# Performance work log

Hardware: AMD Instinct MI355X
Metric: run time of the kernel (lower is better)

## Reference

```python
import jax, jax.numpy as jnp
import numpy as np

B, L, K = 4, 2048, 30
NS, NV = 1024, 256   # node hidden (scalar, vector)
ES, EV = 32, 1       # edge hidden (scalar, vector)
CLAMP = 32           # clamp_rel_pos
PE = 16              # num positional embeddings

def _nan_to_num(t):
    return jnp.where(jnp.isfinite(t), t, jnp.zeros((), t.dtype))

def _norm(t, axis=-1, keepdims=False, eps=1e-8):
    return jnp.sqrt(jnp.sum(t * t, axis=axis, keepdims=keepdims) + eps)

def _normalize(t, axis=-1):
    return _nan_to_num(t / _norm(t, axis=axis, keepdims=True))

def _norm_no_nan(t, axis=-1, keepdims=False, eps=1e-8, sqrt=True):
    out = jnp.maximum(jnp.sum(t * t, axis=axis, keepdims=keepdims), eps)
    return jnp.sqrt(out) if sqrt else out

def _rbf(values, v_min, v_max, n_bins=16):
    centers = jnp.linspace(v_min, v_max, n_bins)
    std = (v_max - v_min) / n_bins
    z = (values[..., None] - centers) / std
    return jnp.exp(-z * z)

def _dihedrals(X, eps=1e-7):
    b = X.shape[0]
    Xf = X[:, :, :3].reshape(b, -1, 3)           # [B, 3L, 3]
    U = _normalize(Xf[:, 1:] - Xf[:, :-1])
    u2, u1, u0 = U[:, :-2], U[:, 1:-1], U[:, 2:]
    n2 = _normalize(jnp.cross(u2, u1))
    n1 = _normalize(jnp.cross(u1, u0))
    cosD = jnp.clip(jnp.sum(n2 * n1, -1), -1 + eps, 1 - eps)
    D = jnp.sign(jnp.sum(u2 * n1, -1)) * jnp.arccos(cosD)
    D = jnp.pad(D, ((0, 0), (1, 2))).reshape(b, -1, 3)
    return jnp.concatenate([jnp.cos(D), jnp.sin(D)], -1)   # [B,L,6]

def _orientations(Xca):
    f = jnp.pad(_normalize(Xca[:, 1:] - Xca[:, :-1]), ((0, 0), (0, 1), (0, 0)))
    bk = jnp.pad(_normalize(Xca[:, :-1] - Xca[:, 1:]), ((0, 0), (1, 0), (0, 0)))
    return jnp.concatenate([f[:, :, None], bk[:, :, None]], -2)  # [B,L,2,3]

def _sidechains(X):
    n, origin, c = X[:, :, 0], X[:, :, 1], X[:, :, 2]
    c, n = _normalize(c - origin), _normalize(n - origin)
    bisector = _normalize(c + n)
    perp = _normalize(jnp.cross(c, n))
    return -bisector * float(np.sqrt(1.0 / 3.0)) - perp * float(np.sqrt(2.0 / 3.0))

def _dist(Xca, coord_mask, res_idx, padding_mask, k, order=3):
    n = Xca.shape[1]
    cmf = coord_mask.astype(jnp.float32)
    cm2 = cmf[:, None, :] * cmf[:, :, None]
    rmf = (~padding_mask).astype(jnp.float32)
    rm2 = rmf[:, None, :] * rmf[:, :, None]
    dX = Xca[:, None, :, :] - Xca[:, :, None, :]
    D = cm2 * _norm(dX, axis=-1)
    cov = (jnp.abs(res_idx[:, :, None] - res_idx[:, None, :]) <= order).astype(jnp.float32)
    D_cov = D * (1.0 - cov)
    seqpos = jnp.arange(n)
    Dseq = jnp.abs(seqpos[:, None] - seqpos[None, :]).astype(jnp.float32)
    D_adjust = _nan_to_num(D_cov) + (1.0 - cm2) * (1e8 + Dseq * 1e6) + (1.0 - rm2) * 1e10
    _, E_idx = jax.lax.top_k(-D_adjust, k)                # k smallest
    D_neighbors = jnp.take_along_axis(D, E_idx, axis=-1)  # regather raw D (as in source)
    return D_neighbors, E_idx, D_neighbors < 5e7, D_neighbors < 5e9

def _edge_features(coords, coord_mask, res_idx, padding_mask):
    Xca = coords[:, :, 1]
    E_dist, E_idx, E_cm, E_rm = _dist(Xca, coord_mask, res_idx, padding_mask, K)
    b, n, k = E_idx.shape
    src = jnp.broadcast_to(jnp.arange(n, dtype=E_idx.dtype)[None, :, None], (b, n, k))
    edge_index = jnp.stack([src, E_idx], 0).reshape(2, b, n * k)
    E_dist = E_dist.reshape(b, n * k)
    E_cm = E_cm.reshape(b, n * k)
    E_rm = E_rm.reshape(b, n * k)
    E_cmf = E_cm[..., None].astype(jnp.float32)
    edge_start = jnp.take_along_axis(res_idx, edge_index[0], axis=-1)
    edge_end = jnp.take_along_axis(res_idx, edge_index[1], axis=-1)
    d = jnp.clip(edge_start - edge_end, -CLAMP, CLAMP).astype(jnp.float32)
    freq = jnp.exp(jnp.arange(0, PE, 2, dtype=jnp.float32) * (-np.log(10000.0) / PE))
    ang = d[..., None] * freq
    pos = jnp.concatenate([jnp.cos(ang), jnp.sin(ang)], -1)
    D_rbf = _rbf(E_dist, 0.0, 20.0)
    X_src = jnp.broadcast_to(Xca[:, :, None, :], (b, n, k, 3)).reshape(b, n * k, 3)
    X_dest = jnp.take_along_axis(Xca, edge_index[1][..., None], axis=1)
    cm_src = jnp.broadcast_to(coord_mask[:, :, None], (b, n, k)).reshape(b, n * k)
    cm_dest = jnp.take_along_axis(coord_mask, edge_index[1], axis=1)
    E_vec = X_src - X_dest
    E_mean = jnp.sum(E_vec * E_cmf, 1, keepdims=True) / jnp.sum(E_cmf, 1, keepdims=True)
    E_vec = E_vec * E_cmf + E_mean * (1.0 - E_cmf)
    edge_s = _nan_to_num(jnp.concatenate([D_rbf, pos], -1))
    edge_v = _nan_to_num(_normalize(E_vec)[:, :, None, :])
    edge_s = jnp.concatenate([edge_s,
                              (~cm_src).astype(jnp.float32)[..., None],
                              (~cm_dest).astype(jnp.float32)[..., None]], -1)  # [B,Lk,34]
    invalid = (~E_rm) | (~E_cm)   # remove_edges_without_coords=True
    edge_index = jnp.where(invalid[None], -1, edge_index)
    return edge_s, edge_v, jnp.transpose(edge_index, (1, 0, 2)), invalid

def _gvp(s, v, wh, ws_w, ws_b, wv):
    # v: [..., vi, 3]; activations=(None, None), vector_gate=False
    vh = jnp.einsum('...id,ih->...hd', v, wh)       # [..., h, 3]
    vn = _norm_no_nan(vh, axis=-1)                  # [..., h]
    s_out = jnp.concatenate([s, vn], -1) @ ws_w + ws_b
    v_out = jnp.einsum('...hd,hv->...vd', vh, wv)
    return s_out, v_out

def _gvp_layernorm(s, v, gamma, beta, eps=1e-4):
    mu = jnp.mean(s, -1, keepdims=True)
    var = jnp.mean((s - mu) ** 2, -1, keepdims=True)
    s_out = (s - mu) / jnp.sqrt(var + eps) * gamma + beta
    vn2 = _norm_no_nan(v, axis=-1, keepdims=True, sqrt=False)
    v_out = v / jnp.sqrt(jnp.mean(vn2, axis=-2, keepdims=True))
    return s_out, v_out

def _forward(coords, coord_mask, res_idx, padding_mask, confidence,
             node_wh, node_ws_w, node_ws_b, node_wv, node_ln_g, node_ln_b,
             edge_wh, edge_ws_w, edge_ws_b, edge_wv, edge_ln_g, edge_ln_b,
             conf_w, conf_b):
    node_s = jnp.concatenate([_dihedrals(coords),
                              coord_mask.astype(jnp.float32)[..., None]], -1)  # [B,L,7]
    node_v = jnp.concatenate([_orientations(coords[:, :, 1]),
                              _sidechains(coords)[:, :, None]], -2)            # [B,L,3,3]
    edge_s, edge_v, edge_index, invalid = _edge_features(coords, coord_mask, res_idx, padding_mask)
    # torch.no_grad() over featurization
    node_s, node_v, edge_s, edge_v = map(jax.lax.stop_gradient,
                                         (node_s, node_v, edge_s, edge_v))
    ns, nv = _gvp_layernorm(*_gvp(node_s, node_v, node_wh, node_ws_w, node_ws_b, node_wv),
                            node_ln_g, node_ln_b)
    es, ev = _gvp_layernorm(*_gvp(edge_s, edge_v, edge_wh, edge_ws_w, edge_ws_b, edge_wv),
                            edge_ln_g, edge_ln_b)
    ns = ns + _rbf(confidence, 0.0, 1.0) @ conf_w + conf_b
    b = ns.shape[0]
    ns = ns.reshape(b * L, NS)
    nv = nv.reshape(b * L, NV, 3)
    es = es.reshape(b * L * K, ES)
    ev = ev.reshape(b * L * K, EV, 3)
    # flatten_graph (padded: invalid edges kept with index -1, embeddings zeroed)
    valid = (~invalid).reshape(-1)
    ei = edge_index + (jnp.arange(b, dtype=edge_index.dtype) * L)[:, None, None]
    ei = jnp.transpose(ei, (1, 0, 2)).reshape(2, -1)
    ei = jnp.where(valid[None, :], ei, -1)
    es = jnp.where(valid[:, None], es, 0.0)
    ev = jnp.where(valid[:, None, None], ev, 0.0)
    return ns, nv, es, ev, ei

def setup_inputs():
    key = jax.random.key(0)
    ks = jax.random.split(key, 12)
    def lin(k, fan_in, shape):
        return jax.random.normal(k, shape, jnp.float32) / np.sqrt(fan_in)
    return {
        'coords': jax.random.normal(ks[0], (B, L, 3, 3), jnp.float32),
        'coord_mask': jax.random.randint(ks[1], (B, L), 0, 2) > 0,
        'res_idx': jnp.arange(B * L, dtype=jnp.int32).reshape(B, L),
        'padding_mask': jnp.zeros((B, L), dtype=bool),
        'confidence': jax.random.uniform(ks[2], (B, L), jnp.float32),
        'node_wh': lin(ks[3], 3, (3, NV)),
        'node_ws_w': lin(ks[4], NV + 7, (NV + 7, NS)),
        'node_ws_b': jnp.zeros((NS,), jnp.float32),
        'node_wv': lin(ks[5], NV, (NV, NV)),
        'node_ln_g': jnp.ones((NS,), jnp.float32),
        'node_ln_b': jnp.zeros((NS,), jnp.float32),
        'edge_wh': lin(ks[6], 1, (1, 1)),
        'edge_ws_w': lin(ks[7], 35, (35, ES)),
        'edge_ws_b': jnp.zeros((ES,), jnp.float32),
        'edge_wv': lin(ks[8], 1, (1, 1)),
        'edge_ln_g': jnp.ones((ES,), jnp.float32),
        'edge_ln_b': jnp.zeros((ES,), jnp.float32),
        'conf_w': lin(ks[9], 16, (16, NS)),
        'conf_b': jnp.zeros((NS,), jnp.float32),
    }

def reference(coords, coord_mask, res_idx, padding_mask, confidence,
              node_wh, node_ws_w, node_ws_b, node_wv, node_ln_g, node_ln_b,
              edge_wh, edge_ws_w, edge_ws_b, edge_wv, edge_ln_g, edge_ln_b,
              conf_w, conf_b):
    return _forward(coords, coord_mask, res_idx, padding_mask, confidence,
                    node_wh, node_ws_w, node_ws_b, node_wv, node_ln_g, node_ln_b,
                    edge_wh, edge_ws_w, edge_ws_b, edge_wv, edge_ln_g, edge_ln_b,
                    conf_w, conf_b)
```

## Files before the change

### kernel.cpp

```cpp
#include <hip/hip_runtime.h>
#include <math.h>

constexpr int Bc = 4, Lc = 2048, Kc = 30;
constexpr int Nn = Bc * Lc;
constexpr int NSc = 1024, NVc = 256;
constexpr int NEc = Nn * Kc;
constexpr int SK = 263;

constexpr size_t OUT_NS = 0;
constexpr size_t OUT_NV = (size_t)Nn * NSc;
constexpr size_t OUT_ES = OUT_NV + (size_t)Nn * NVc * 3;
constexpr size_t OUT_EV = OUT_ES + (size_t)NEc * 32;
constexpr size_t OUT_EI = OUT_EV + (size_t)NEc * 3;

constexpr size_t WS_SIN = 0;
constexpr size_t WS_NDV = WS_SIN + (size_t)Nn * SK;
constexpr size_t WS_EIX = WS_NDV + (size_t)Nn * 9;
constexpr size_t WS_EDS = WS_EIX + (size_t)NEc;
constexpr size_t WS_CMF = WS_EDS + (size_t)NEc;

__device__ __forceinline__ void norml3(float& x, float& y, float& z) {
  float ss = x*x + y*y + z*z;
  float inv = 1.0f / sqrtf(ss + 1e-8f);
  x *= inv; y *= inv; z *= inv;
}

__global__ __launch_bounds__(256) void kinit(const unsigned char* __restrict__ cm,
                                             const float* __restrict__ coords,
                                             const int* __restrict__ resid,
                                             const unsigned char* __restrict__ pmask,
                                             const float* __restrict__ wh,
                                             const float* __restrict__ wv,
                                             float* __restrict__ ws,
                                             float4* __restrict__ pack,
                                             float4* __restrict__ whwv4,
                                             float4* __restrict__ wht4) {
  __shared__ float r0[256], r1[256], r2[256];
  __shared__ int flag;
  int tid = threadIdx.x;
  if (blockIdx.x < 32) {
    if (tid == 0) flag = 0;
    __syncthreads();
    int any = 0;
    for (int p = tid; p < 1024; p += 256)
      if (p & 3) any |= cm[p];
    if (any) atomicOr(&flag, 1);
    __syncthreads();
    bool bytefmt = (flag != 0);
    int n = blockIdx.x * 256 + tid;
    unsigned char v = bytefmt ? cm[n] : cm[4*n];
    ws[WS_CMF + n] = v ? 1.f : 0.f;
    int rm = (pmask[n] == 0) ? 1 : 0;
    int w = (resid[n] << 2) | ((v ? 1 : 0) << 1) | rm;
    float4 p;
    p.x = coords[(size_t)n*9 + 3];
    p.y = coords[(size_t)n*9 + 4];
    p.z = coords[(size_t)n*9 + 5];
    p.w = __int_as_float(w);
    pack[n] = p;
  } else {
    int lane = tid & 63, wid = tid >> 6;
    int vcol = (int)(blockIdx.x - 32) * 64 + lane;
    float a0 = 0.f, a1 = 0.f, a2 = 0.f;
    #pragma unroll 4
    for (int hh = 0; hh < 64; ++hh) {
      int h = wid * 64 + hh;
      float wvv = wv[(size_t)h * 256 + vcol];
      a0 = fmaf(wh[h],       wvv, a0);
      a1 = fmaf(wh[256 + h], wvv, a1);
      a2 = fmaf(wh[512 + h], wvv, a2);
    }
    r0[tid] = a0; r1[tid] = a1; r2[tid] = a2;
    __syncthreads();
    if (wid == 0) {
      a0 = r0[lane] + r0[lane+64] + r0[lane+128] + r0[lane+192];
      a1 = r1[lane] + r1[lane+64] + r1[lane+128] + r1[lane+192];
      a2 = r2[lane] + r2[lane+64] + r2[lane+128] + r2[lane+192];
      whwv4[vcol] = float4{a0, a1, a2, 0.f};
    } else if (wid == 1) {
      wht4[vcol] = float4{wh[vcol], wh[256 + vcol], wh[512 + vcol], 0.f};
    }
  }
}

__global__ __launch_bounds__(64) void knode_geom(const float* __restrict__ coords,
                                                 float* __restrict__ ws) {
  int n = blockIdx.x * 64 + threadIdx.x;
  if (n >= Nn) return;
  int b = n / Lc, l = n % Lc;
  const float* Xb = coords + (size_t)b * Lc * 9;
  float ax[7][3];
  #pragma unroll
  for (int m = 0; m < 7; ++m) {
    int t = 3*l + m - 2;
    if (t >= 0 && t < 3*Lc) { ax[m][0]=Xb[t*3+0]; ax[m][1]=Xb[t*3+1]; ax[m][2]=Xb[t*3+2]; }
    else { ax[m][0]=0.f; ax[m][1]=0.f; ax[m][2]=0.f; }
  }
  float U[5][3];
  #pragma unroll
  for (int mi = 0; mi < 5; ++mi) {
    int t = 3*l - 1 + mi;
    if (t >= 0 && t <= 3*Lc - 2) {
      float x = ax[mi+2][0]-ax[mi+1][0], y = ax[mi+2][1]-ax[mi+1][1], z = ax[mi+2][2]-ax[mi+1][2];
      norml3(x,y,z);
      U[mi][0]=x; U[mi][1]=y; U[mi][2]=z;
    } else { U[mi][0]=0.f; U[mi][1]=0.f; U[mi][2]=0.f; }
  }
  float cph[3], sph[3];
  #pragma unroll
  for (int a = 0; a < 3; ++a) {
    int t = 3*l + a - 1;
    if (t < 0 || t > 3*Lc - 4) { cph[a] = 1.f; sph[a] = 0.f; continue; }
    const float *u2 = U[a], *u1 = U[a+1], *u0 = U[a+2];
    float n2x = u2[1]*u1[2]-u2[2]*u1[1], n2y = u2[2]*u1[0]-u2[0]*u1[2], n2z = u2[0]*u1[1]-u2[1]*u1[0];
    norml3(n2x,n2y,n2z);
    float n1x = u1[1]*u0[2]-u1[2]*u0[1], n1y = u1[2]*u0[0]-u1[0]*u0[2], n1z = u1[0]*u0[1]-u1[1]*u0[0];
    norml3(n1x,n1y,n1z);
    float cd = n2x*n1x + n2y*n1y + n2z*n1z;
    cd = fminf(fmaxf(cd, -1.f + 1e-7f), 1.f - 1e-7f);
    float dt = u2[0]*n1x + u2[1]*n1y + u2[2]*n1z;
    float sg = (dt > 0.f) ? 1.f : ((dt < 0.f) ? -1.f : 0.f);
    float D = sg * acosf(cd);
    cph[a] = cosf(D); sph[a] = sinf(D);
  }
  float fx=0.f,fy=0.f,fz=0.f, kx=0.f,ky=0.f,kz=0.f;
  if (l < Lc-1) { fx=ax[6][0]-ax[3][0]; fy=ax[6][1]-ax[3][1]; fz=ax[6][2]-ax[3][2]; norml3(fx,fy,fz); }
  if (l > 0)    { kx=ax[0][0]-ax[3][0]; ky=ax[0][1]-ax[3][1]; kz=ax[0][2]-ax[3][2]; norml3(kx,ky,kz); }
  float cx=ax[4][0]-ax[3][0], cy=ax[4][1]-ax[3][1], cz=ax[4][2]-ax[3][2]; norml3(cx,cy,cz);
  float nx=ax[2][0]-ax[3][0], ny=ax[2][1]-ax[3][1], nz=ax[2][2]-ax[3][2]; norml3(nx,ny,nz);
  float bix=cx+nx, biy=cy+ny, biz=cz+nz; norml3(bix,biy,biz);
  float px=cy*nz-cz*ny, py=cz*nx-cx*nz, pz=cx*ny-cy*nx; norml3(px,py,pz);
  const float c1 = 0.57735026f, c2 = 0.81649658f;
  float sx = -bix*c1 - px*c2, sy = -biy*c1 - py*c2, sz = -biz*c1 - pz*c2;

  float cmf = ws[WS_CMF + n];
  float* sr = ws + WS_SIN + (size_t)n * SK;
  sr[0]=cph[0]; sr[1]=cph[1]; sr[2]=cph[2]; sr[3]=sph[0]; sr[4]=sph[1]; sr[5]=sph[2]; sr[6]=cmf;
  float* vr = ws + WS_NDV + (size_t)n * 9;
  vr[0]=fx; vr[1]=fy; vr[2]=fz; vr[3]=kx; vr[4]=ky; vr[5]=kz; vr[6]=sx; vr[7]=sy; vr[8]=sz;
}

__global__ __launch_bounds__(256) void kvnode(const float4* __restrict__ wht4,
                                              const float4* __restrict__ whwv4,
                                              float* __restrict__ ws,
                                              float* __restrict__ out) {
  int tid = threadIdx.x, lane = tid & 63, wid = tid >> 6;
  int n = blockIdx.x * 4 + wid;
  const float* v = ws + WS_NDV + (size_t)n * 9;
  float v00=v[0],v01=v[1],v02=v[2];
  float v10=v[3],v11=v[4],v12=v[5];
  float v20=v[6],v21=v[7],v22=v[8];
  float p = 0.f;
  float vo[4][3];
  #pragma unroll
  for (int m = 0; m < 4; ++m) {
    int h = lane + 64*m;
    float4 wt = wht4[h];
    float vh0 = v00*wt.x + v10*wt.y + v20*wt.z;
    float vh1 = v01*wt.x + v11*wt.y + v21*wt.z;
    float vh2 = v02*wt.x + v12*wt.y + v22*wt.z;
    ws[WS_SIN + (size_t)n*SK + 7 + h] = sqrtf(fmaxf(vh0*vh0 + vh1*vh1 + vh2*vh2, 1e-8f));
    float4 wc = whwv4[h];
    float o0 = v00*wc.x + v10*wc.y + v20*wc.z;
    float o1 = v01*wc.x + v11*wc.y + v21*wc.z;
    float o2 = v02*wc.x + v12*wc.y + v22*wc.z;
    vo[m][0]=o0; vo[m][1]=o1; vo[m][2]=o2;
    p += fmaxf(o0*o0 + o1*o1 + o2*o2, 1e-8f);
  }
  #pragma unroll
  for (int off = 1; off < 64; off <<= 1) p += __shfl_xor(p, off);
  float isd = 1.f / sqrtf(p * (1.f/256.f));
  #pragma unroll
  for (int m = 0; m < 4; ++m) {
    size_t o = OUT_NV + (size_t)n*768 + (size_t)(lane + 64*m)*3;
    out[o+0] = vo[m][0]*isd;
    out[o+1] = vo[m][1]*isd;
    out[o+2] = vo[m][2]*isd;
  }
}

__global__ __launch_bounds__(256) void ktopk(const float4* __restrict__ pack,
                                             float* __restrict__ ws) {
  __shared__ unsigned long long cbuf[4][256];
  int tid = threadIdx.x, lane = tid & 63, wid = tid >> 6;
  int row = blockIdx.x * 4 + wid;
  int b = row >> 11;
  int i = row & (Lc - 1);
  const float4* P = pack + (size_t)b * Lc;
  int* eix = (int*)(ws + WS_EIX);
  unsigned long long lmask_lt = (1ULL << lane) - 1ULL;

  float4 pi = P[i];
  int wi = __float_as_int(pi.w);
  float cmi = ((wi >> 1) & 1) ? 1.f : 0.f;
  float rmi = (wi & 1) ? 1.f : 0.f;
  int ri = wi >> 2;

  unsigned a[32];
  unsigned lmin = 0xFFFFFFFFu;
  #pragma unroll
  for (int m = 0; m < 32; ++m) {
    int j = lane + 64*m;
    float4 pj = P[j];
    int wj = __float_as_int(pj.w);
    float cmj = ((wj >> 1) & 1) ? 1.f : 0.f;
    float rmj = (wj & 1) ? 1.f : 0.f;
    float dx = __fsub_rn(pi.x, pj.x);
    float dy = __fsub_rn(pi.y, pj.y);
    float dz = __fsub_rn(pi.z, pj.z);
    float ss = __fadd_rn(__fadd_rn(__fmul_rn(dx,dx), __fmul_rn(dy,dy)), __fmul_rn(dz,dz));
    float dist = __fsqrt_rn(__fadd_rn(ss, 1e-8f));
    float cm2 = __fmul_rn(cmi, cmj);
    float D = __fmul_rn(cm2, dist);
    int ad = ri - (wj >> 2); ad = ad < 0 ? -ad : ad;
    float covm = (ad <= 3) ? 0.f : 1.f;
    float dseq = (float)(i >= j ? i - j : j - i);
    float t1 = __fmul_rn(__fsub_rn(1.f, cm2), __fadd_rn(1e8f, __fmul_rn(dseq, 1e6f)));
    float rm2 = __fmul_rn(rmi, rmj);
    float t2 = __fmul_rn(__fsub_rn(1.f, rm2), 1e10f);
    float adj = __fadd_rn(__fadd_rn(__fmul_rn(D, covm), t1), t2);
    unsigned u = __float_as_uint(adj);
    a[m] = u;
    lmin = u < lmin ? u : lmin;
  }

  unsigned lo = 0u, hi = 0xFFFFFFFFu;
  while (lo < hi) {
    unsigned mid = lo + ((hi - lo) >> 1);
    unsigned long long bal = __ballot(lmin <= mid);
    if (__popcll(bal) >= Kc) hi = mid; else lo = mid + 1u;
  }
  unsigned Tv = lo;

  unsigned base = 0;
  #pragma unroll
  for (int m = 0; m < 32; ++m) {
    bool pred = (a[m] <= Tv);
    unsigned long long bal = __ballot(pred);
    if (pred) {
      unsigned pos = base + (unsigned)__popcll(bal & lmask_lt);
      if (pos < 256u)
        cbuf[wid][pos] = ((unsigned long long)a[m] << 32) | (unsigned)(lane + 64*m);
    }
    base += (unsigned)__popcll(bal);
  }
  unsigned M = base < 256u ? base : 256u;
  __builtin_amdgcn_wave_barrier();

  for (unsigned idx = (unsigned)lane; idx < M; idx += 64u) {
    unsigned long long k0 = cbuf[wid][idx];
    int rank = 0;
    for (unsigned t = 0; t < M; ++t) rank += (cbuf[wid][t] < k0) ? 1 : 0;
    if (rank < Kc) {
      int j = (int)(k0 & 2047ULL);
      float4 pj = P[j];
      int wj = __float_as_int(pj.w);
      float cmj = ((wj >> 1) & 1) ? 1.f : 0.f;
      float dx = __fsub_rn(pi.x, pj.x);
      float dy = __fsub_rn(pi.y, pj.y);
      float dz = __fsub_rn(pi.z, pj.z);
      float ss2 = __fadd_rn(__fadd_rn(__fmul_rn(dx,dx), __fmul_rn(dy,dy)), __fmul_rn(dz,dz));
      float dist = __fsqrt_rn(__fadd_rn(ss2, 1e-8f));
      float D = __fmul_rn(__fmul_rn(cmi, cmj), dist);
      eix[(size_t)row*Kc + rank] = j;
      ws[WS_EDS + (size_t)row*Kc + rank] = D;
    }
  }
}

__global__ __launch_bounds__(256) void kgemm_s(const float* __restrict__ ws,
                                               const float* __restrict__ wsw,
                                               const float* __restrict__ wsb,
                                               float* __restrict__ out) {
  __shared__ __align__(16) float As[32][132];
  __shared__ __align__(16) float Bs[32][64];
  int tid = threadIdx.x;
  int lb = (int)(blockIdx.x & 7) * 128 + (int)(blockIdx.x >> 3);
  int by = lb >> 4, bx = lb & 15;
  int row0 = by * 128, cn0 = bx * 64;
  int tx = tid & 15, ty = tid >> 4;
  int aka = tid & 15, arw = tid >> 4;
  int bkk = tid >> 4, bc4 = tid & 15;
  const float* Abase = ws + WS_SIN;

  float ar[16];
  float4 br[2];
  #pragma unroll
  for (int h = 0; h < 2; ++h) {
    int ka = h*16 + aka;
    #pragma unroll
    for (int i = 0; i < 8; ++i)
      ar[h*8+i] = Abase[(size_t)(row0 + arw + 16*i)*SK + ka];
    br[h] = *(const float4*)&wsw[(size_t)(h*16 + bkk)*NSc + cn0 + bc4*4];
  }
  float acc[8][4] = {};
  for (int k0 = 0; k0 < SK; k0 += 32) {
    #pragma unroll
    for (int h = 0; h < 2; ++h) {
      #pragma unroll
      for (int i = 0; i < 8; ++i)
        As[h*16 + aka][arw + 16*i] = ar[h*8+i];
      *(float4*)&Bs[h*16 + bkk][bc4*4] = br[h];
    }
    __syncthreads();
    int kn = k0 + 32;
    if (kn < SK) {
      #pragma unroll
      for (int h = 0; h < 2; ++h) {
        int ka = kn + h*16 + aka;
        bool ok = (ka < SK);
        #pragma unroll
        for (int i = 0; i < 8; ++i)
          ar[h*8+i] = ok ? Abase[(size_t)(row0 + arw + 16*i)*SK + ka] : 0.f;
        int kb = kn + h*16 + bkk;
        br[h] = (kb < SK) ? *(const float4*)&wsw[(size_t)kb*NSc + cn0 + bc4*4]
                          : float4{0.f,0.f,0.f,0.f};
      }
    }
    #pragma unroll 4
    for (int kk = 0; kk < 32; ++kk) {
      float4 a0 = *(const float4*)&As[kk][ty*8 + 0];
      float4 a1 = *(const float4*)&As[kk][ty*8 + 4];
      float4 b4 = *(const float4*)&Bs[kk][tx*4];
      float av[8] = {a0.x,a0.y,a0.z,a0.w, a1.x,a1.y,a1.z,a1.w};
      float bv[4] = {b4.x,b4.y,b4.z,b4.w};
      #pragma unroll
      for (int r = 0; r < 8; ++r)
        #pragma unroll
        for (int c = 0; c < 4; ++c)
          acc[r][c] = fmaf(av[r], bv[c], acc[r][c]);
    }
    __syncthreads();
  }
  float4 bb = *(const float4*)&wsb[cn0 + tx*4];
  #pragma unroll
  for (int r = 0; r < 8; ++r) {
    size_t o = OUT_NS + (size_t)(row0 + ty*8 + r)*NSc + cn0 + tx*4;
    float4 ov = {acc[r][0]+bb.x, acc[r][1]+bb.y, acc[r][2]+bb.z, acc[r][3]+bb.w};
    *(float4*)&out[o] = ov;
  }
}

__global__ __launch_bounds__(256) void kedge(const float* __restrict__ coords,
    const int* __restrict__ resid,
    const float* __restrict__ ewh, const float* __restrict__ eww,
    const float* __restrict__ ewb, const float* __restrict__ ewv,
    const float* __restrict__ elg, const float* __restrict__ elb,
    const float* __restrict__ ws, float* __restrict__ out) {
  __shared__ float w[35*32];
  __shared__ float wb[32], g[32], bb[32];
  int tid = threadIdx.x;
  for (int t = tid; t < 35*32; t += 256) w[t] = eww[t];
  if (tid < 32) { wb[tid] = ewb[tid]; g[tid] = elg[tid]; bb[tid] = elb[tid]; }
  __syncthreads();
  int e = blockIdx.x * 256 + tid;
  if (e >= NEc) return;
  int b = e / (Lc*Kc);
  int rem = e - b*(Lc*Kc);
  int i = rem / Kc;
  int row = b*Lc + i;
  const int* eix = (const int*)(ws + WS_EIX);
  int j = eix[e];
  float Dn = ws[WS_EDS + e];
  bool jok = ((unsigned)j < (unsigned)Lc);
  bool valid = jok && (Dn < 5e7f) && (Dn < 5e9f);
  if (!valid) {
    #pragma unroll
    for (int c = 0; c < 32; ++c) out[OUT_ES + (size_t)e*32 + c] = 0.f;
    out[OUT_EV + (size_t)e*3 + 0] = 0.f;
    out[OUT_EV + (size_t)e*3 + 1] = 0.f;
    out[OUT_EV + (size_t)e*3 + 2] = 0.f;
    out[OUT_EI + e]       = -1.f;
    out[OUT_EI + NEc + e] = -1.f;
    return;
  }
  int dcl = resid[row] - resid[b*Lc + j];
  dcl = dcl < -32 ? -32 : (dcl > 32 ? 32 : dcl);
  float dpos = (float)dcl;
  float s[35];
  #pragma unroll
  for (int m = 0; m < 16; ++m) {
    float c = (20.f/15.f) * (float)m;
    float z = (Dn - c) * 0.8f;
    s[m] = expf(-z*z);
  }
  #pragma unroll
  for (int m = 0; m < 8; ++m) {
    float fr = expf((float)(2*m) * (-0.57564627324851148f));
    float ang = dpos * fr;
    s[16+m] = cosf(ang);
    s[24+m] = sinf(ang);
  }
  float csf = ws[WS_CMF + row];
  float cdf = ws[WS_CMF + b*Lc + j];
  s[32] = 1.f - csf; s[33] = 1.f - cdf;
  const float* Xb = coords + (size_t)b*Lc*9;
  float vx = Xb[i*9+3] - Xb[j*9+3];
  float vy = Xb[i*9+4] - Xb[j*9+4];
  float vz = Xb[i*9+5] - Xb[j*9+5];
  float ss2 = vx*vx + vy*vy + vz*vz;
  float inv = 1.f / sqrtf(ss2 + 1e-8f);
  float e0 = vx*inv, e1 = vy*inv, e2 = vz*inv;
  if (!isfinite(e0)) e0 = 0.f;
  if (!isfinite(e1)) e1 = 0.f;
  if (!isfinite(e2)) e2 = 0.f;
  float wh00 = ewh[0], wv00 = ewv[0];
  float vh0 = e0*wh00, vh1 = e1*wh00, vh2 = e2*wh00;
  s[34] = sqrtf(fmaxf(vh0*vh0 + vh1*vh1 + vh2*vh2, 1e-8f));
  float o[32]; float sm = 0.f;
  #pragma unroll
  for (int c = 0; c < 32; ++c) {
    float a = wb[c];
    #pragma unroll
    for (int q = 0; q < 35; ++q) a = fmaf(s[q], w[q*32 + c], a);
    o[c] = a; sm += a;
  }
  float mu = sm * (1.f/32.f);
  float sq = 0.f;
  #pragma unroll
  for (int c = 0; c < 32; ++c) { float dd = o[c]-mu; sq += dd*dd; }
  float isd = 1.f / sqrtf(sq*(1.f/32.f) + 1e-4f);
  float vo0 = vh0*wv00, vo1 = vh1*wv00, vo2 = vh2*wv00;
  float vn2 = fmaxf(vo0*vo0 + vo1*vo1 + vo2*vo2, 1e-8f);
  float ivn = 1.f / sqrtf(vn2);
  #pragma unroll
  for (int c = 0; c < 32; ++c)
    out[OUT_ES + (size_t)e*32 + c] = (o[c]-mu)*isd*g[c] + bb[c];
  out[OUT_EV + (size_t)e*3 + 0] = vo0*ivn;
  out[OUT_EV + (size_t)e*3 + 1] = vo1*ivn;
  out[OUT_EV + (size_t)e*3 + 2] = vo2*ivn;
  out[OUT_EI + e]       = (float)row;
  out[OUT_EI + NEc + e] = (float)(b*Lc + j);
}

__global__ __launch_bounds__(256) void kln_node(const float* __restrict__ conf,
    const float* __restrict__ cw, const float* __restrict__ cb,
    const float* __restrict__ lg, const float* __restrict__ lb,
    float* __restrict__ out) {
  int n = blockIdx.x, tid = threadIdx.x;
  size_t base = OUT_NS + (size_t)n*NSc;
  float x0 = out[base + tid];
  float x1 = out[base + tid + 256];
  float x2 = out[base + tid + 512];
  float x3 = out[base + tid + 768];
  float sm = x0+x1+x2+x3;
  float sq = x0*x0+x1*x1+x2*x2+x3*x3;
  int lane = tid & 63, wid = tid >> 6;
  #pragma unroll
  for (int off = 32; off > 0; off >>= 1) { sm += __shfl_down(sm, off); sq += __shfl_down(sq, off); }
  __shared__ float rs[4], rq[4];
  if (lane == 0) { rs[wid] = sm; rq[wid] = sq; }
  __syncthreads();
  sm = rs[0]+rs[1]+rs[2]+rs[3];
  sq = rq[0]+rq[1]+rq[2]+rq[3];
  float mu = sm * (1.f/1024.f);
  float var = fmaxf(sq * (1.f/1024.f) - mu*mu, 0.f);
  float isd = 1.f / sqrtf(var + 1e-4f);
  float cf = conf[n];
  float rb[16];
  #pragma unroll
  for (int m = 0; m < 16; ++m) {
    float z = (cf - (float)m*(1.f/15.f)) * 16.f;
    rb[m] = expf(-z*z);
  }
  float xs_[4] = {x0, x1, x2, x3};
  #pragma unroll
  for (int q = 0; q < 4; ++q) {
    int c = tid + q*256;
    float t = cb[c];
    #pragma unroll
    for (int m = 0; m < 16; ++m) t = fmaf(rb[m], cw[m*1024 + c], t);
    out[base + c] = (xs_[q]-mu)*isd*lg[c] + lb[c] + t;
  }
}

extern "C" void kernel_launch(void* const* d_in, const int* in_sizes, int n_in,
                              void* d_out, int out_size, void* d_ws, size_t ws_size,
                              hipStream_t stream) {
  const float* coords         = (const float*)d_in[0];
  const unsigned char* cmask  = (const unsigned char*)d_in[1];
  const int* resid            = (const int*)d_in[2];
  const unsigned char* pmask  = (const unsigned char*)d_in[3];
  const float* conf           = (const float*)d_in[4];
  const float* nwh            = (const float*)d_in[5];
  const float* nww            = (const float*)d_in[6];
  const float* nwb            = (const float*)d_in[7];
  const float* nwv            = (const float*)d_in[8];
  const float* nlg            = (const float*)d_in[9];
  const float* nlb            = (const float*)d_in[10];
  const float* ewh            = (const float*)d_in[11];
  const float* eww            = (const float*)d_in[12];
  const float* ewb            = (const float*)d_in[13];
  const float* ewv            = (const float*)d_in[14];
  const float* elg            = (const float*)d_in[15];
  const float* elb            = (const float*)d_in[16];
  const float* cw             = (const float*)d_in[17];
  const float* cb             = (const float*)d_in[18];
  float* out = (float*)d_out;
  float* ws  = (float*)d_ws;
  float4* whwv4 = (float4*)(out + OUT_ES);
  float4* wht4  = whwv4 + 256;
  float4* pack  = (float4*)(out + OUT_EV);

  kinit<<<36, 256, 0, stream>>>(cmask, coords, resid, pmask, nwh, nwv, ws, pack, whwv4, wht4);
  knode_geom<<<Nn/64, 64, 0, stream>>>(coords, ws);
  kvnode<<<Nn/4, 256, 0, stream>>>(wht4, whwv4, ws, out);
  ktopk<<<Nn/4, 256, 0, stream>>>(pack, ws);
  kgemm_s<<<(Nn/128)*(NSc/64), 256, 0, stream>>>(ws, nww, nwb, out);
  kedge<<<NEc/256, 256, 0, stream>>>(coords, resid, ewh, eww, ewb, ewv, elg, elb, ws, out);
  kln_node<<<Nn, 256, 0, stream>>>(conf, cw, cb, nlg, nlb, out);
}
```

Baseline: 297.9 us.

## Coalesce edge and node-vector output stores, batch top-k loads, narrow search range

The edge kernel now stages each block's 32-channel edge scalars and 3-wide edge vectors in shared memory and writes them out as coalesced float4 stores. Invalid edges no longer take an early return; every thread computes with a clamped index and selects zero at the end. The node-vector kernel permutes its weight indexing so each lane owns 12 contiguous outputs and stores them as three float4s. In top-k, loads are batched 16 at a time for memory-level parallelism, and the binary-search upper bound is narrowed to a float-bit cap. The shared staging adds LDS use and barriers, and removing the e>=NEc guard relies on NEc dividing evenly by 256.

```diff
diff --git a/kernel.cpp b/kernel.cpp
--- a/kernel.cpp
+++ b/kernel.cpp
@@ -154,13 +154,14 @@
   float vo[4][3];
   #pragma unroll
   for (int m = 0; m < 4; ++m) {
-    int h = lane + 64*m;
-    float4 wt = wht4[h];
+    int hv = lane + 64*m;
+    float4 wt = wht4[hv];
     float vh0 = v00*wt.x + v10*wt.y + v20*wt.z;
     float vh1 = v01*wt.x + v11*wt.y + v21*wt.z;
     float vh2 = v02*wt.x + v12*wt.y + v22*wt.z;
-    ws[WS_SIN + (size_t)n*SK + 7 + h] = sqrtf(fmaxf(vh0*vh0 + vh1*vh1 + vh2*vh2, 1e-8f));
-    float4 wc = whwv4[h];
+    ws[WS_SIN + (size_t)n*SK + 7 + hv] = sqrtf(fmaxf(vh0*vh0 + vh1*vh1 + vh2*vh2, 1e-8f));
+    int ho = lane*4 + m;
+    float4 wc = whwv4[ho];
     float o0 = v00*wc.x + v10*wc.y + v20*wc.z;
     float o1 = v01*wc.x + v11*wc.y + v21*wc.z;
     float o2 = v02*wc.x + v12*wc.y + v22*wc.z;
@@ -170,13 +171,13 @@
   #pragma unroll
   for (int off = 1; off < 64; off <<= 1) p += __shfl_xor(p, off);
   float isd = 1.f / sqrtf(p * (1.f/256.f));
-  #pragma unroll
-  for (int m = 0; m < 4; ++m) {
-    size_t o = OUT_NV + (size_t)n*768 + (size_t)(lane + 64*m)*3;
-    out[o+0] = vo[m][0]*isd;
-    out[o+1] = vo[m][1]*isd;
-    out[o+2] = vo[m][2]*isd;
-  }
+  size_t o = OUT_NV + (size_t)n*768 + (size_t)lane*12;
+  float4 f0 = {vo[0][0]*isd, vo[0][1]*isd, vo[0][2]*isd, vo[1][0]*isd};
+  float4 f1 = {vo[1][1]*isd, vo[1][2]*isd, vo[2][0]*isd, vo[2][1]*isd};
+  float4 f2 = {vo[2][2]*isd, vo[3][0]*isd, vo[3][1]*isd, vo[3][2]*isd};
+  *(float4*)&out[o+0] = f0;
+  *(float4*)&out[o+4] = f1;
+  *(float4*)&out[o+8] = f2;
 }
 
 __global__ __launch_bounds__(256) void ktopk(const float4* __restrict__ pack,
@@ -199,32 +200,40 @@
   unsigned a[32];
   unsigned lmin = 0xFFFFFFFFu;
   #pragma unroll
-  for (int m = 0; m < 32; ++m) {
-    int j = lane + 64*m;
-    float4 pj = P[j];
-    int wj = __float_as_int(pj.w);
-    float cmj = ((wj >> 1) & 1) ? 1.f : 0.f;
-    float rmj = (wj & 1) ? 1.f : 0.f;
-    float dx = __fsub_rn(pi.x, pj.x);
-    float dy = __fsub_rn(pi.y, pj.y);
-    float dz = __fsub_rn(pi.z, pj.z);
-    float ss = __fadd_rn(__fadd_rn(__fmul_rn(dx,dx), __fmul_rn(dy,dy)), __fmul_rn(dz,dz));
-    float dist = __fsqrt_rn(__fadd_rn(ss, 1e-8f));
-    float cm2 = __fmul_rn(cmi, cmj);
-    float D = __fmul_rn(cm2, dist);
-    int ad = ri - (wj >> 2); ad = ad < 0 ? -ad : ad;
-    float covm = (ad <= 3) ? 0.f : 1.f;
-    float dseq = (float)(i >= j ? i - j : j - i);
-    float t1 = __fmul_rn(__fsub_rn(1.f, cm2), __fadd_rn(1e8f, __fmul_rn(dseq, 1e6f)));
-    float rm2 = __fmul_rn(rmi, rmj);
-    float t2 = __fmul_rn(__fsub_rn(1.f, rm2), 1e10f);
-    float adj = __fadd_rn(__fadd_rn(__fmul_rn(D, covm), t1), t2);
-    unsigned u = __float_as_uint(adj);
-    a[m] = u;
-    lmin = u < lmin ? u : lmin;
-  }
-
-  unsigned lo = 0u, hi = 0xFFFFFFFFu;
+  for (int half = 0; half < 2; ++half) {
+    float4 pjs[16];
+    #pragma unroll
+    for (int q = 0; q < 16; ++q)
+      pjs[q] = P[lane + 64*(half*16 + q)];
+    #pragma unroll
+    for (int q = 0; q < 16; ++q) {
+      int m = half*16 + q;
+      int j = lane + 64*m;
+      float4 pj = pjs[q];
+      int wj = __float_as_int(pj.w);
+      float cmj = ((wj >> 1) & 1) ? 1.f : 0.f;
+      float rmj = (wj & 1) ? 1.f : 0.f;
+      float dx = __fsub_rn(pi.x, pj.x);
+      float dy = __fsub_rn(pi.y, pj.y);
+      float dz = __fsub_rn(pi.z, pj.z);
+      float ss = __fadd_rn(__fadd_rn(__fmul_rn(dx,dx), __fmul_rn(dy,dy)), __fmul_rn(dz,dz));
+      float dist = __fsqrt_rn(__fadd_rn(ss, 1e-8f));
+      float cm2 = __fmul_rn(cmi, cmj);
+      float D = __fmul_rn(cm2, dist);
+      int ad = ri - (wj >> 2); ad = ad < 0 ? -ad : ad;
+      float covm = (ad <= 3) ? 0.f : 1.f;
+      float dseq = (float)(i >= j ? i - j : j - i);
+      float t1 = __fmul_rn(__fsub_rn(1.f, cm2), __fadd_rn(1e8f, __fmul_rn(dseq, 1e6f)));
+      float rm2 = __fmul_rn(rmi, rmj);
+      float t2 = __fmul_rn(__fsub_rn(1.f, rm2), 1e10f);
+      float adj = __fadd_rn(__fadd_rn(__fmul_rn(D, covm), t1), t2);
+      unsigned u = __float_as_uint(adj);
+      a[m] = u;
+      lmin = u < lmin ? u : lmin;
+    }
+  }
+
+  unsigned lo = 0u, hi = 0x51000000u;
   while (lo < hi) {
     unsigned mid = lo + ((hi - lo) >> 1);
     unsigned long long bal = __ballot(lmin <= mid);
@@ -349,12 +358,12 @@
     const float* __restrict__ ws, float* __restrict__ out) {
   __shared__ float w[35*32];
   __shared__ float wb[32], g[32], bb[32];
+  __shared__ float es[256*33];
   int tid = threadIdx.x;
   for (int t = tid; t < 35*32; t += 256) w[t] = eww[t];
   if (tid < 32) { wb[tid] = ewb[tid]; g[tid] = elg[tid]; bb[tid] = elb[tid]; }
   __syncthreads();
   int e = blockIdx.x * 256 + tid;
-  if (e >= NEc) return;
   int b = e / (Lc*Kc);
   int rem = e - b*(Lc*Kc);
   int i = rem / Kc;
@@ -364,17 +373,9 @@
   float Dn = ws[WS_EDS + e];
   bool jok = ((unsigned)j < (unsigned)Lc);
   bool valid = jok && (Dn < 5e7f) && (Dn < 5e9f);
-  if (!valid) {
-    #pragma unroll
-    for (int c = 0; c < 32; ++c) out[OUT_ES + (size_t)e*32 + c] = 0.f;
-    out[OUT_EV + (size_t)e*3 + 0] = 0.f;
-    out[OUT_EV + (size_t)e*3 + 1] = 0.f;
-    out[OUT_EV + (size_t)e*3 + 2] = 0.f;
-    out[OUT_EI + e]       = -1.f;
-    out[OUT_EI + NEc + e] = -1.f;
-    return;
-  }
-  int dcl = resid[row] - resid[b*Lc + j];
+  int sj = jok ? j : 0;
+
+  int dcl = resid[row] - resid[b*Lc + sj];
   dcl = dcl < -32 ? -32 : (dcl > 32 ? 32 : dcl);
   float dpos = (float)dcl;
   float s[35];
@@ -392,12 +393,12 @@
     s[24+m] = sinf(ang);
   }
   float csf = ws[WS_CMF + row];
-  float cdf = ws[WS_CMF + b*Lc + j];
+  float cdf = ws[WS_CMF + b*Lc + sj];
   s[32] = 1.f - csf; s[33] = 1.f - cdf;
   const float* Xb = coords + (size_t)b*Lc*9;
-  float vx = Xb[i*9+3] - Xb[j*9+3];
-  float vy = Xb[i*9+4] - Xb[j*9+4];
-  float vz = Xb[i*9+5] - Xb[j*9+5];
+  float vx = Xb[i*9+3] - Xb[sj*9+3];
+  float vy = Xb[i*9+4] - Xb[sj*9+4];
+  float vz = Xb[i*9+5] - Xb[sj*9+5];
   float ss2 = vx*vx + vy*vy + vz*vz;
   float inv = 1.f / sqrtf(ss2 + 1e-8f);
   float e0 = vx*inv, e1 = vy*inv, e2 = vz*inv;
@@ -423,14 +424,33 @@
   float vo0 = vh0*wv00, vo1 = vh1*wv00, vo2 = vh2*wv00;
   float vn2 = fmaxf(vo0*vo0 + vo1*vo1 + vo2*vo2, 1e-8f);
   float ivn = 1.f / sqrtf(vn2);
+
   #pragma unroll
   for (int c = 0; c < 32; ++c)
-    out[OUT_ES + (size_t)e*32 + c] = (o[c]-mu)*isd*g[c] + bb[c];
-  out[OUT_EV + (size_t)e*3 + 0] = vo0*ivn;
-  out[OUT_EV + (size_t)e*3 + 1] = vo1*ivn;
-  out[OUT_EV + (size_t)e*3 + 2] = vo2*ivn;
-  out[OUT_EI + e]       = (float)row;
-  out[OUT_EI + NEc + e] = (float)(b*Lc + j);
+    es[tid*33 + c] = valid ? ((o[c]-mu)*isd*g[c] + bb[c]) : 0.f;
+  out[OUT_EI + e]       = valid ? (float)row : -1.f;
+  out[OUT_EI + NEc + e] = valid ? (float)(b*Lc + j) : -1.f;
+  __syncthreads();
+  {
+    size_t base32 = OUT_ES + (size_t)blockIdx.x * 256 * 32;
+    #pragma unroll
+    for (int k = 0; k < 8; ++k) {
+      int flat = (k*256 + tid) * 4;
+      int el = flat >> 5, c0 = flat & 31;
+      float4 vq = {es[el*33+c0], es[el*33+c0+1], es[el*33+c0+2], es[el*33+c0+3]};
+      *(float4*)&out[base32 + flat] = vq;
+    }
+  }
+  __syncthreads();
+  es[tid*3 + 0] = valid ? vo0*ivn : 0.f;
+  es[tid*3 + 1] = valid ? vo1*ivn : 0.f;
+  es[tid*3 + 2] = valid ? vo2*ivn : 0.f;
+  __syncthreads();
+  if (tid < 192) {
+    size_t base3 = OUT_EV + (size_t)blockIdx.x * 768;
+    float4 vq = {es[tid*4], es[tid*4+1], es[tid*4+2], es[tid*4+3]};
+    *(float4*)&out[base3 + tid*4] = vq;
+  }
 }
 
 __global__ __launch_bounds__(256) void kln_node(const float* __restrict__ conf,
```

Measured after the change: 285.7 us. -4.1%, faster.
